# Kernel tuning notes

Measured on AMD Instinct MI355X. Metric: run time of the kernel, lower is better.

## Reference

```python
import jax, jax.numpy as jnp
import numpy as np

P, F_IN, HG, C, T, E, HOUT = 4096, 64, 64, 64, 32, 65536, 12
LEAKY_SLOPE = 0.2
LN_EPS = 1e-5


def setup_inputs() -> dict:
    key = jax.random.key(0)
    ks = jax.random.split(key, 14)
    g = lambda k, shape, scale: (jax.random.normal(k, shape, jnp.float32) * scale)
    return {
        "X": jax.random.normal(ks[0], (1, P, F_IN, T), jnp.float32),
        "edge_index": jax.random.randint(ks[1], (T, 2, E), 0, P, jnp.int32),
        # GATv2 params (single head)
        "Wl": g(ks[2], (F_IN, HG), 0.1),
        "Wr": g(ks[3], (F_IN, HG), 0.1),
        "att": g(ks[4], (HG,), 0.1),
        "gat_b": g(ks[5], (HG,), 0.02),
        # 1x1 time conv (HG -> C) and 1x1 residual conv (F_IN -> C)
        "W_time": g(ks[6], (C, HG), 0.1),
        "b_time": g(ks[7], (C,), 0.02),
        "W_res": g(ks[8], (C, F_IN), 0.1),
        "b_res": g(ks[9], (C,), 0.02),
        # LayerNorm over channel dim C
        "ln_g": jnp.ones((C,), jnp.float32),
        "ln_b": jnp.zeros((C,), jnp.float32),
        # final conv: Conv2d(in=T, out=HOUT, kernel=(1, C)) -> weight (HOUT, T, C)
        "W_final": g(ks[10], (HOUT, T, C), 0.05),
        "b_final": g(ks[11], (HOUT,), 0.02),
    }


def reference(X, edge_index, Wl, Wr, att, gat_b, W_time, b_time, W_res, b_res,
              ln_g, ln_b, W_final, b_final):
    Pn = X.shape[1]

    def gat_t(x, edges):
        # x: (P, F_IN), edges: (2, E) with edges[0]=src j, edges[1]=dst i
        src, dst = edges[0], edges[1]
        hl = x @ Wl                      # (P, HG) messages
        hr = x @ Wr                      # (P, HG) query side
        e = jax.nn.leaky_relu(hl[src] + hr[dst], LEAKY_SLOPE) @ att  # (E,)
        emax = jax.ops.segment_max(e, dst, num_segments=Pn)
        ex = jnp.exp(e - emax[dst])
        den = jax.ops.segment_sum(ex, dst, num_segments=Pn)
        alpha = ex / den[dst]            # softmax over in-edges of each dst
        return jax.ops.segment_sum(alpha[:, None] * hl[src], dst,
                                   num_segments=Pn) + gat_b  # (P, HG)

    xs = jnp.moveaxis(X[0], -1, 0)                     # (T, P, F_IN)
    X_hat = jax.nn.relu(jax.vmap(gat_t)(xs, edge_index))  # (T, P, HG)

    th = jnp.einsum('tph,ch->tpc', X_hat, W_time) + b_time  # time conv 1x1
    rs = jnp.einsum('tpf,cf->tpc', xs, W_res) + b_res       # residual conv 1x1
    y = jax.nn.relu(th + rs)                                 # (T, P, C)

    mu = jnp.mean(y, axis=-1, keepdims=True)
    var = jnp.var(y, axis=-1, keepdims=True)
    yn = (y - mu) * jax.lax.rsqrt(var + LN_EPS) * ln_g + ln_b  # (T, P, C)

    # final conv: in-channels = T, kernel (1, C) -> contract over t and c
    out = jnp.einsum('tpc,otc->po', yn, W_final) + b_final     # (P, HOUT)
    return out[None]                                           # (1, P, HOUT)
```

## Files before the change

### kernel.cpp

```cpp
#include <hip/hip_runtime.h>
#include <math.h>

#define NP 4096
#define F_IN 64
#define HG 64
#define NC 64
#define NT 32
#define NE 65536
#define HOUT 12
#define LEAKY 0.2f
#define LN_EPS 1e-5f
#define CAP 48

template <int CTRL>
__device__ __forceinline__ float dppadd(float v, float x) {
    int r = __builtin_amdgcn_update_dpp(0, __builtin_bit_cast(int, x), CTRL, 0xF, 0xF, false);
    return v + __builtin_bit_cast(float, r);
}
__device__ __forceinline__ float rowsum16(float v) {
    v = dppadd<0x128>(v, v);
    v = dppadd<0x124>(v, v);
    v = dppadd<0x122>(v, v);
    v = dppadd<0x121>(v, v);
    return v;
}
__device__ __forceinline__ float laneXorSum(float v) {
    v += __shfl_xor(v, 16, 64);
    v += __shfl_xor(v, 32, 64);
    return v;
}

#define FMA4(Acomp, B, r)                                                     \
    acc[r][0] += (Acomp) * (B).x; acc[r][1] += (Acomp) * (B).y;               \
    acc[r][2] += (Acomp) * (B).z; acc[r][3] += (Acomp) * (B).w;

__global__ __launch_bounds__(256) void k_front(const float* __restrict__ X,
        const float* __restrict__ Wl, const float* __restrict__ Wr,
        const float* __restrict__ W_res, const float* __restrict__ b_res,
        const float* __restrict__ W_time, const float* __restrict__ bf,
        float* __restrict__ hl, float* __restrict__ hr, float* __restrict__ rs,
        float* __restrict__ wtT, float* __restrict__ out,
        int* __restrict__ cnt) {
    __shared__ float smem[8960];
    int b = blockIdx.x;
    int tid = threadIdx.x;
    if (b < 2048) {
        float (*xs)[F_IN][36] = (float (*)[F_IN][36])smem;
        float (*bk)[68] = (float (*)[68])(smem + 4608);
        int p0 = b * 2;
        const float4* Xp = (const float4*)(X + (size_t)p0 * F_IN * NT);
        for (int i4 = tid; i4 < 1024; i4 += 256) {
            int pp = i4 >> 9, f = (i4 >> 3) & 63, t0 = (i4 & 7) * 4;
            *(float4*)&xs[pp][f][t0] = Xp[i4];
        }
        int ng = tid & 15, pp = (tid >> 4) & 1, tg = tid >> 5;
        int n0 = ng * 4, t0 = tg * 4;
        {
            const float4* B4 = (const float4*)Wl;
            for (int i4 = tid; i4 < 1024; i4 += 256)
                *(float4*)&bk[i4 >> 4][(i4 & 15) * 4] = B4[i4];
            __syncthreads();
            float acc[4][4];
#pragma unroll
            for (int i = 0; i < 4; ++i)
#pragma unroll
                for (int j2 = 0; j2 < 4; ++j2) acc[i][j2] = 0.f;
#pragma unroll 8
            for (int f = 0; f < F_IN; ++f) {
                float4 B = *(const float4*)&bk[f][n0];
                float4 A = *(const float4*)&xs[pp][f][t0];
                FMA4(A.x, B, 0) FMA4(A.y, B, 1) FMA4(A.z, B, 2) FMA4(A.w, B, 3)
            }
#pragma unroll
            for (int i = 0; i < 4; ++i) {
                float4 v;
                v.x = acc[i][0]; v.y = acc[i][1]; v.z = acc[i][2]; v.w = acc[i][3];
                *(float4*)&hl[((size_t)(t0 + i) * NP + p0 + pp) * HG + n0] = v;
            }
            __syncthreads();
        }
        {
            const float4* B4 = (const float4*)Wr;
            for (int i4 = tid; i4 < 1024; i4 += 256)
                *(float4*)&bk[i4 >> 4][(i4 & 15) * 4] = B4[i4];
            __syncthreads();
            float acc[4][4];
#pragma unroll
            for (int i = 0; i < 4; ++i)
#pragma unroll
                for (int j2 = 0; j2 < 4; ++j2) acc[i][j2] = 0.f;
#pragma unroll 8
            for (int f = 0; f < F_IN; ++f) {
                float4 B = *(const float4*)&bk[f][n0];
                float4 A = *(const float4*)&xs[pp][f][t0];
                FMA4(A.x, B, 0) FMA4(A.y, B, 1) FMA4(A.z, B, 2) FMA4(A.w, B, 3)
            }
#pragma unroll
            for (int i = 0; i < 4; ++i) {
                float4 v;
                v.x = acc[i][0]; v.y = acc[i][1]; v.z = acc[i][2]; v.w = acc[i][3];
                *(float4*)&hr[((size_t)(t0 + i) * NP + p0 + pp) * HG + n0] = v;
            }
            __syncthreads();
        }
        {
            for (int i = tid; i < F_IN * NC; i += 256) {
                int c = i >> 6, f = i & 63;
                bk[f][c] = W_res[i];
            }
            __syncthreads();
            float4 br4 = *(const float4*)&b_res[n0];
            float acc[4][4];
#pragma unroll
            for (int i = 0; i < 4; ++i) {
                acc[i][0] = br4.x; acc[i][1] = br4.y; acc[i][2] = br4.z; acc[i][3] = br4.w;
            }
#pragma unroll 8
            for (int f = 0; f < F_IN; ++f) {
                float4 B = *(const float4*)&bk[f][n0];
                float4 A = *(const float4*)&xs[pp][f][t0];
                FMA4(A.x, B, 0) FMA4(A.y, B, 1) FMA4(A.z, B, 2) FMA4(A.w, B, 3)
            }
#pragma unroll
            for (int i = 0; i < 4; ++i) {
                float4 v;
                v.x = acc[i][0]; v.y = acc[i][1]; v.z = acc[i][2]; v.w = acc[i][3];
                *(float4*)&rs[((size_t)(t0 + i) * NP + p0 + pp) * NC + n0] = v;
            }
        }
    } else if (b < 2064) {
        int i = (b - 2048) * 256 + tid;
        wtT[i] = W_time[(i & 63) * 64 + (i >> 6)];
    } else if (b < 2256) {
        int i = (b - 2064) * 256 + tid;
        out[i] = bf[i % HOUT];
    } else {
        int4 z = {0, 0, 0, 0};
        ((int4*)cnt)[(b - 2256) * 256 + tid] = z;
    }
}

__global__ __launch_bounds__(256) void k_scatter(const int* __restrict__ EI,
        int* __restrict__ cnt, unsigned short* __restrict__ scap) {
    int b = blockIdx.x;
    int j = b >> 3;
    int t = (b & 7) + 8 * (j & 3);
    int c = j >> 2;
    int tid = threadIdx.x;
    const int4* srcA = (const int4*)(EI + (size_t)t * 2 * NE) + c * (NE / 128);
    const int4* dstA = (const int4*)(EI + (size_t)t * 2 * NE + NE) + c * (NE / 128);
    int* cntT = cnt + (t << 12);
    unsigned short* scT = scap + ((size_t)t << 12) * CAP;
    for (int i = tid; i < NE / 128; i += 256) {
        int4 s = srcA[i];
        int4 d = dstA[i];
        int sl;
        sl = atomicAdd(&cntT[d.x], 1); if (sl < CAP) scT[d.x * CAP + sl] = (unsigned short)s.x;
        sl = atomicAdd(&cntT[d.y], 1); if (sl < CAP) scT[d.y * CAP + sl] = (unsigned short)s.y;
        sl = atomicAdd(&cntT[d.z], 1); if (sl < CAP) scT[d.z * CAP + sl] = (unsigned short)s.z;
        sl = atomicAdd(&cntT[d.w], 1); if (sl < CAP) scT[d.w * CAP + sl] = (unsigned short)s.w;
    }
}

__global__ __launch_bounds__(256) void k_gat(const float* __restrict__ hl,
        float* __restrict__ hr,
        const int* __restrict__ cnt, const unsigned short* __restrict__ scap,
        const float* __restrict__ att, const float* __restrict__ gat_b) {
    __shared__ int sidx[4][64];
    int b = blockIdx.x;
    int k = b >> 3;
    int t = (b & 7) + 8 * (k >> 10);
    int ws = threadIdx.x >> 6;
    int i = (k & 1023) * 4 + ws;
    int lane = threadIdx.x & 63;
    int row = lane >> 4;
    int c0 = (lane & 15) * 4;
    size_t nbase = ((size_t)t * NP + i) * HG;
    const float* hlt = hl + (size_t)t * NP * HG;
    float4 r4 = *(const float4*)&hr[nbase + c0];
    float4 at4 = *(const float4*)&att[c0];
    int deg = cnt[(t << 12) + i];
    deg = (deg < CAP) ? deg : CAP;
    const unsigned short* sp = scap + ((size_t)((t << 12) + i)) * CAP;
    int stage = (lane < deg) ? lane : 0;
    sidx[ws][lane] = (int)sp[stage];
    float l = 0.f;
    float4 acc = {0.f, 0.f, 0.f, 0.f};
    int nfull = deg & ~7;
    int j = 0;
    for (; j < nfull; j += 8) {
        int src0 = sidx[ws][j + row];
        int src1 = sidx[ws][j + 4 + row];
        float4 h0 = *(const float4*)&hlt[((size_t)src0 << 6) + c0];
        float4 h1 = *(const float4*)&hlt[((size_t)src1 << 6) + c0];
        float4 z0, z1;
        z0.x = h0.x + r4.x; z0.y = h0.y + r4.y; z0.z = h0.z + r4.z; z0.w = h0.w + r4.w;
        z1.x = h1.x + r4.x; z1.y = h1.y + r4.y; z1.z = h1.z + r4.z; z1.w = h1.w + r4.w;
        z0.x = fmaxf(z0.x, LEAKY * z0.x); z0.y = fmaxf(z0.y, LEAKY * z0.y);
        z0.z = fmaxf(z0.z, LEAKY * z0.z); z0.w = fmaxf(z0.w, LEAKY * z0.w);
        z1.x = fmaxf(z1.x, LEAKY * z1.x); z1.y = fmaxf(z1.y, LEAKY * z1.y);
        z1.z = fmaxf(z1.z, LEAKY * z1.z); z1.w = fmaxf(z1.w, LEAKY * z1.w);
        float e0 = rowsum16(z0.x * at4.x + z0.y * at4.y + z0.z * at4.z + z0.w * at4.w);
        float e1 = rowsum16(z1.x * at4.x + z1.y * at4.y + z1.z * at4.z + z1.w * at4.w);
        float w0 = __expf(e0);
        float w1 = __expf(e1);
        l += w0 + w1;
        acc.x += w0 * h0.x + w1 * h1.x;
        acc.y += w0 * h0.y + w1 * h1.y;
        acc.z += w0 * h0.z + w1 * h1.z;
        acc.w += w0 * h0.w + w1 * h1.w;
    }
    for (; j < deg; j += 4) {
        int jj = j + row;
        int src = sidx[ws][(jj < deg) ? jj : 0];
        float4 ha = *(const float4*)&hlt[((size_t)src << 6) + c0];
        float4 za;
        za.x = ha.x + r4.x; za.y = ha.y + r4.y; za.z = ha.z + r4.z; za.w = ha.w + r4.w;
        za.x = fmaxf(za.x, LEAKY * za.x);
        za.y = fmaxf(za.y, LEAKY * za.y);
        za.z = fmaxf(za.z, LEAKY * za.z);
        za.w = fmaxf(za.w, LEAKY * za.w);
        float ep = za.x * at4.x + za.y * at4.y + za.z * at4.z + za.w * at4.w;
        float e = rowsum16(ep);
        float w = __expf(e);
        w = (jj < deg) ? w : 0.f;
        l += w;
        acc.x += w * ha.x; acc.y += w * ha.y; acc.z += w * ha.z; acc.w += w * ha.w;
    }
    float lt = laneXorSum(l);
    acc.x = laneXorSum(acc.x);
    acc.y = laneXorSum(acc.y);
    acc.z = laneXorSum(acc.z);
    acc.w = laneXorSum(acc.w);
    if (row == 0) {
        float inv = (deg > 0) ? (1.0f / lt) : 0.f;
        float4 gb = *(const float4*)&gat_b[c0];
        float4 o;
        o.x = fmaxf(acc.x * inv + gb.x, 0.f);
        o.y = fmaxf(acc.y * inv + gb.y, 0.f);
        o.z = fmaxf(acc.z * inv + gb.z, 0.f);
        o.w = fmaxf(acc.w * inv + gb.w, 0.f);
        *(float4*)&hr[nbase + c0] = o;
    }
}

__global__ __launch_bounds__(256) void k_pf(const float* __restrict__ Xhat,
        const float* __restrict__ wtT, const float* __restrict__ b_time,
        const float* __restrict__ rs, const float* __restrict__ ln_g,
        const float* __restrict__ ln_b, const float* __restrict__ Wf,
        float* __restrict__ out) {
    __shared__ float in_t[64][68];
    __shared__ float bk[64][68];
    int bx = blockIdx.x;
    int tc = bx & 7;
    int p0 = (bx >> 3) * 64;
    int tid = threadIdx.x;
    const float4* wsrc = (const float4*)wtT;
    for (int i4 = tid; i4 < 1024; i4 += 256) {
        int h = i4 >> 4, c4 = (i4 & 15) * 4;
        *(float4*)&bk[h][c4] = wsrc[i4];
    }
    int cg = tid & 15, pg = tid >> 4;
    int c0 = cg * 4, pl = pg * 4;
    float4 bt4 = *(const float4*)&b_time[c0];
    float4 lg = *(const float4*)&ln_g[c0];
    float4 lb = *(const float4*)&ln_b[c0];
    float ot[4][HOUT];
#pragma unroll
    for (int i = 0; i < 4; ++i)
#pragma unroll
        for (int o = 0; o < HOUT; ++o) ot[i][o] = 0.f;
    for (int ti = 0; ti < 4; ++ti) {
        int t = tc + ti * 8;
        __syncthreads();
        const float4* src = (const float4*)(Xhat + ((size_t)t * NP + p0) * HG);
        for (int i4 = tid; i4 < 1024; i4 += 256) {
            int pp = i4 >> 4, c4 = (i4 & 15) * 4;
            *(float4*)&in_t[pp][c4] = src[i4];
        }
        __syncthreads();
        float acc[4][4];
#pragma unroll
        for (int i = 0; i < 4; ++i) {
            acc[i][0] = bt4.x; acc[i][1] = bt4.y; acc[i][2] = bt4.z; acc[i][3] = bt4.w;
        }
#pragma unroll
        for (int k4 = 0; k4 < 16; ++k4) {
            float4 A0 = *(const float4*)&in_t[pl + 0][k4 * 4];
            float4 A1 = *(const float4*)&in_t[pl + 1][k4 * 4];
            float4 A2 = *(const float4*)&in_t[pl + 2][k4 * 4];
            float4 A3 = *(const float4*)&in_t[pl + 3][k4 * 4];
            float4 B0 = *(const float4*)&bk[k4 * 4 + 0][c0];
            FMA4(A0.x, B0, 0) FMA4(A1.x, B0, 1) FMA4(A2.x, B0, 2) FMA4(A3.x, B0, 3)
            float4 B1 = *(const float4*)&bk[k4 * 4 + 1][c0];
            FMA4(A0.y, B1, 0) FMA4(A1.y, B1, 1) FMA4(A2.y, B1, 2) FMA4(A3.y, B1, 3)
            float4 B2 = *(const float4*)&bk[k4 * 4 + 2][c0];
            FMA4(A0.z, B2, 0) FMA4(A1.z, B2, 1) FMA4(A2.z, B2, 2) FMA4(A3.z, B2, 3)
            float4 B3 = *(const float4*)&bk[k4 * 4 + 3][c0];
            FMA4(A0.w, B3, 0) FMA4(A1.w, B3, 1) FMA4(A2.w, B3, 2) FMA4(A3.w, B3, 3)
        }
        float4 ynv[4];
#pragma unroll
        for (int i = 0; i < 4; ++i) {
            size_t prow = (size_t)t * NP + p0 + pl + i;
            float4 r4 = *(const float4*)&rs[prow * NC + c0];
            float y0 = fmaxf(acc[i][0] + r4.x, 0.f), y1 = fmaxf(acc[i][1] + r4.y, 0.f);
            float y2 = fmaxf(acc[i][2] + r4.z, 0.f), y3 = fmaxf(acc[i][3] + r4.w, 0.f);
            float s = rowsum16(y0 + y1 + y2 + y3);
            float ss = rowsum16(y0 * y0 + y1 * y1 + y2 * y2 + y3 * y3);
            float mu = s * (1.f / 64.f);
            float var = ss * (1.f / 64.f) - mu * mu;
            float rsd = rsqrtf(var + LN_EPS);
            ynv[i].x = (y0 - mu) * rsd * lg.x + lb.x;
            ynv[i].y = (y1 - mu) * rsd * lg.y + lb.y;
            ynv[i].z = (y2 - mu) * rsd * lg.z + lb.z;
            ynv[i].w = (y3 - mu) * rsd * lg.w + lb.w;
        }
#pragma unroll
        for (int o = 0; o < HOUT; ++o) {
            float4 w4 = *(const float4*)&Wf[(size_t)o * NT * NC + t * NC + c0];
#pragma unroll
            for (int i = 0; i < 4; ++i)
                ot[i][o] += ynv[i].x * w4.x + ynv[i].y * w4.y
                          + ynv[i].z * w4.z + ynv[i].w * w4.w;
        }
    }
#pragma unroll
    for (int i = 0; i < 4; ++i)
#pragma unroll
        for (int o = 0; o < HOUT; ++o) ot[i][o] = rowsum16(ot[i][o]);
    if (cg == 0) {
#pragma unroll
        for (int i = 0; i < 4; ++i) {
            int p = p0 + pl + i;
#pragma unroll
            for (int o = 0; o < HOUT; ++o)
                atomicAdd(&out[p * HOUT + o], ot[i][o]);
        }
    }
}

extern "C" void kernel_launch(void* const* d_in, const int* in_sizes, int n_in,
                              void* d_out, int out_size, void* d_ws, size_t ws_size,
                              hipStream_t stream) {
    const float* X      = (const float*)d_in[0];
    const int*   EI     = (const int*)d_in[1];
    const float* Wl     = (const float*)d_in[2];
    const float* Wr     = (const float*)d_in[3];
    const float* att    = (const float*)d_in[4];
    const float* gat_b  = (const float*)d_in[5];
    const float* W_time = (const float*)d_in[6];
    const float* b_time = (const float*)d_in[7];
    const float* W_res  = (const float*)d_in[8];
    const float* b_res  = (const float*)d_in[9];
    const float* ln_g   = (const float*)d_in[10];
    const float* ln_b   = (const float*)d_in[11];
    const float* Wf     = (const float*)d_in[12];
    const float* bf     = (const float*)d_in[13];
    float* out = (float*)d_out;

    char* ws = (char*)d_ws;
    const size_t MB = 1024 * 1024;
    float* hl   = (float*)(ws);
    float* hr   = (float*)(ws + 32 * MB);
    float* rs   = (float*)(ws + 64 * MB);
    int*   cnt  = (int*)  (ws + 96 * MB);
    float* wtT  = (float*)(ws + 96 * MB + 512 * 1024);
    unsigned short* scap = (unsigned short*)(ws + 97 * MB);

    k_front  <<<2384, 256, 0, stream>>>(X, Wl, Wr, W_res, b_res, W_time, bf,
                                        hl, hr, rs, wtT, out, cnt);
    k_scatter<<<1024, 256, 0, stream>>>(EI, cnt, scap);
    k_gat    <<<(NT * NP) / 4, 256, 0, stream>>>(hl, hr, cnt, scap, att, gat_b);
    k_pf     <<<512, 256, 0, stream>>>(hr, wtT, b_time, rs, ln_g, ln_b, Wf, out);
}
```

Baseline: 334.0 us.

## Build per-destination edge buckets in LDS instead of global atomics

Replaces the global-atomic edge scatter with a kernel in which each block owns 512 destination nodes of one timestep. The block scans all edges of that timestep, bins the matching ones into a shared-memory bucket array with LDS atomics, then writes counts and buckets to global memory with coalesced stores. This removes the global atomics and the zeroing of the count array in the front kernel. In exchange, every block re-reads the whole edge list of its timestep, so edge reads grow eightfold, and the grid shrinks to 256 blocks using about 50KB of LDS each.

New measurement: 283.5 us. 15.1% less time.

```diff
diff --git a/kernel.cpp b/kernel.cpp
--- a/kernel.cpp
+++ b/kernel.cpp
@@ -39,8 +39,7 @@
         const float* __restrict__ W_res, const float* __restrict__ b_res,
         const float* __restrict__ W_time, const float* __restrict__ bf,
         float* __restrict__ hl, float* __restrict__ hr, float* __restrict__ rs,
-        float* __restrict__ wtT, float* __restrict__ out,
-        int* __restrict__ cnt) {
+        float* __restrict__ wtT, float* __restrict__ out) {
     __shared__ float smem[8960];
     int b = blockIdx.x;
     int tid = threadIdx.x;
@@ -131,35 +130,38 @@
     } else if (b < 2064) {
         int i = (b - 2048) * 256 + tid;
         wtT[i] = W_time[(i & 63) * 64 + (i >> 6)];
-    } else if (b < 2256) {
+    } else {
         int i = (b - 2064) * 256 + tid;
         out[i] = bf[i % HOUT];
-    } else {
-        int4 z = {0, 0, 0, 0};
-        ((int4*)cnt)[(b - 2256) * 256 + tid] = z;
-    }
-}
-
-__global__ __launch_bounds__(256) void k_scatter(const int* __restrict__ EI,
+    }
+}
+
+__global__ __launch_bounds__(512) void k_build(const int* __restrict__ EI,
         int* __restrict__ cnt, unsigned short* __restrict__ scap) {
+    __shared__ unsigned short buck[512][CAP];
+    __shared__ int cnts[512];
     int b = blockIdx.x;
-    int j = b >> 3;
-    int t = (b & 7) + 8 * (j & 3);
-    int c = j >> 2;
+    int t = (b & 7) + 8 * ((b >> 3) & 3);
+    int r = b >> 5;
     int tid = threadIdx.x;
-    const int4* srcA = (const int4*)(EI + (size_t)t * 2 * NE) + c * (NE / 128);
-    const int4* dstA = (const int4*)(EI + (size_t)t * 2 * NE + NE) + c * (NE / 128);
-    int* cntT = cnt + (t << 12);
-    unsigned short* scT = scap + ((size_t)t << 12) * CAP;
-    for (int i = tid; i < NE / 128; i += 256) {
+    cnts[tid] = 0;
+    __syncthreads();
+    const int4* srcA = (const int4*)(EI + (size_t)t * 2 * NE);
+    const int4* dstA = (const int4*)(EI + (size_t)t * 2 * NE + NE);
+    for (int i = tid; i < NE / 4; i += 512) {
         int4 s = srcA[i];
         int4 d = dstA[i];
-        int sl;
-        sl = atomicAdd(&cntT[d.x], 1); if (sl < CAP) scT[d.x * CAP + sl] = (unsigned short)s.x;
-        sl = atomicAdd(&cntT[d.y], 1); if (sl < CAP) scT[d.y * CAP + sl] = (unsigned short)s.y;
-        sl = atomicAdd(&cntT[d.z], 1); if (sl < CAP) scT[d.z * CAP + sl] = (unsigned short)s.z;
-        sl = atomicAdd(&cntT[d.w], 1); if (sl < CAP) scT[d.w * CAP + sl] = (unsigned short)s.w;
-    }
+        if ((d.x >> 9) == r) { int lo = d.x & 511; int sl = atomicAdd(&cnts[lo], 1); if (sl < CAP) buck[lo][sl] = (unsigned short)s.x; }
+        if ((d.y >> 9) == r) { int lo = d.y & 511; int sl = atomicAdd(&cnts[lo], 1); if (sl < CAP) buck[lo][sl] = (unsigned short)s.y; }
+        if ((d.z >> 9) == r) { int lo = d.z & 511; int sl = atomicAdd(&cnts[lo], 1); if (sl < CAP) buck[lo][sl] = (unsigned short)s.z; }
+        if ((d.w >> 9) == r) { int lo = d.w & 511; int sl = atomicAdd(&cnts[lo], 1); if (sl < CAP) buck[lo][sl] = (unsigned short)s.w; }
+    }
+    __syncthreads();
+    cnt[(t << 12) + (r << 9) + tid] = cnts[tid];
+    unsigned int* dstw = (unsigned int*)(scap + ((size_t)((t << 12) + (r << 9))) * CAP);
+    const unsigned int* srcw = (const unsigned int*)buck;
+    for (int i = tid; i < 512 * CAP / 2; i += 512)
+        dstw[i] = srcw[i];
 }
 
 __global__ __launch_bounds__(256) void k_gat(const float* __restrict__ hl,
@@ -368,9 +370,9 @@
     float* wtT  = (float*)(ws + 96 * MB + 512 * 1024);
     unsigned short* scap = (unsigned short*)(ws + 97 * MB);
 
-    k_front  <<<2384, 256, 0, stream>>>(X, Wl, Wr, W_res, b_res, W_time, bf,
-                                        hl, hr, rs, wtT, out, cnt);
-    k_scatter<<<1024, 256, 0, stream>>>(EI, cnt, scap);
-    k_gat    <<<(NT * NP) / 4, 256, 0, stream>>>(hl, hr, cnt, scap, att, gat_b);
-    k_pf     <<<512, 256, 0, stream>>>(hr, wtT, b_time, rs, ln_g, ln_b, Wf, out);
-}
+    k_front<<<2256, 256, 0, stream>>>(X, Wl, Wr, W_res, b_res, W_time, bf,
+                                      hl, hr, rs, wtT, out);
+    k_build<<<256, 512, 0, stream>>>(EI, cnt, scap);
+    k_gat  <<<(NT * NP) / 4, 256, 0, stream>>>(hl, hr, cnt, scap, att, gat_b);
+    k_pf   <<<512, 256, 0, stream>>>(hr, wtT, b_time, rs, ln_g, ln_b, Wf, out);
+}
```
